# Optimization experiments

Measured on AMD Instinct MI355X. Metric: run time of the kernel, lower is better.

Reference implementation:

```python
import jax, jax.numpy as jnp
import numpy as np

N_DATASETS = 2
DATASET_CATS = (1536, 1536)
TOTAL_CATS = 3072
MAX_UNIFY = 1536
N_NODES = TOTAL_CATS + MAX_UNIFY  # 4608
LRELU_ALPHA = 0.2
BI_TEMP = 0.05
NEG_INF = -9e15


def setup_inputs() -> dict:
    key = jax.random.key(0)
    ks = jax.random.split(key, 12)
    nfeat, nfeat_out, nfeat_adj, nhid, nheads = 512, 256, 64, 64, 4
    att_out, mlp = 256, 512
    s = lambda k, sh: (jax.random.normal(k, sh, jnp.float32) * 0.05)
    return {
        'x': jax.random.normal(ks[0], (N_NODES, nfeat), jnp.float32),
        'W_before': s(ks[1], (nfeat, nfeat_out)),
        'b_before': jnp.zeros((nfeat_out,), jnp.float32),
        'W_adj': s(ks[2], (nfeat_out, nfeat_adj)),
        'b_adj': jnp.zeros((nfeat_adj,), jnp.float32),
        'W_heads': s(ks[3], (nheads, nfeat_out, nhid)),
        'a_heads': s(ks[4], (nheads, 2 * nhid)),
        'W_out': s(ks[5], (nheads * nhid, att_out)),
        'a_out': s(ks[6], (2 * att_out,)),
        'W_lin1': s(ks[7], (att_out, mlp)),
        'b_lin1': jnp.zeros((mlp,), jnp.float32),
    }


def _calc_adjacency(x_out, W_adj, b_adj):
    # linear_adj + L2 normalize + cosine similarity + row normalization via diag(1/rowsum)
    af = x_out @ W_adj + b_adj                              # [N, nfeat_adj]
    nrm = jnp.sqrt(jnp.sum(af * af, axis=1, keepdims=True))
    naf = af / jnp.maximum(nrm, 1e-12)
    sim = naf @ naf.T                                       # [N, N]
    rowsum = jnp.sum(sim, axis=1)
    r_inv = 1.0 / rowsum
    r_inv = jnp.where(jnp.isinf(r_inv), 0.0, r_inv)
    return r_inv[:, None] * sim                             # diag(1/rowsum) @ sim


def _gat_multihead(x, adj, W, a):
    # W: [H, F, d], a: [H, 2d]. Standard pyGAT dense attention, vectorized over heads.
    d = W.shape[-1]
    Wh = jnp.einsum('nf,hfd->hnd', x, W)                    # [H, N, d]
    f1 = jnp.einsum('hnd,hd->hn', Wh, a[:, :d])             # [H, N]
    f2 = jnp.einsum('hnd,hd->hn', Wh, a[:, d:])             # [H, N]
    e = jax.nn.leaky_relu(f1[:, :, None] + f2[:, None, :], LRELU_ALPHA)  # [H, N, N]
    att = jnp.where(adj[None] > 0, e, NEG_INF)
    att = jax.nn.softmax(att, axis=-1)
    return jnp.einsum('hnm,hmd->hnd', att, Wh)              # [H, N, d]


def _gat_single(x, adj, W, a):
    d = W.shape[-1]
    Wh = x @ W                                              # [N, d]
    f1 = Wh @ a[:d]
    f2 = Wh @ a[d:]
    e = jax.nn.leaky_relu(f1[:, None] + f2[None, :], LRELU_ALPHA)
    att = jnp.where(adj > 0, e, NEG_INF)
    att = jax.nn.softmax(att, axis=-1)
    return att @ Wh


def reference(x, W_before, b_before, W_adj, b_adj, W_heads, a_heads, W_out, a_out, W_lin1, b_lin1):
    x1 = x @ W_before + b_before                            # linear_before
    adj = _calc_adjacency(x1, W_adj, b_adj)                 # before relu, as in source
    x1 = jax.nn.relu(x1)
    # multi-head GAT layer 1 (concat=True -> elu per head, concat along feature dim)
    h = jax.nn.elu(_gat_multihead(x1, adj, W_heads, a_heads))   # [H, N, d]
    H, N, d = h.shape
    feat = jnp.transpose(h, (1, 0, 2)).reshape(N, H * d)
    x2 = feat + x1                                          # residual; dropout is eval no-op
    # output attention head (concat=False -> no elu inside)
    x3 = jax.nn.elu(_gat_single(x2, adj, W_out, a_out) + x2)
    feat_mlp = x3 @ W_lin1 + b_lin1                          # linear1
    # sep_bipartite_graphs: per-dataset column-softmax over unify columns
    bgs = []
    cur = 0
    for nc in DATASET_CATS:
        blk = adj[cur:cur + nc, TOTAL_CATS:]                 # [nc, MAX_UNIFY]
        bgs.append(jax.nn.softmax(blk / BI_TEMP, axis=0))
        cur += nc
    return (feat_mlp[TOTAL_CATS:],) + tuple(bgs)


if __name__ == '__main__':
    out = reference(**setup_inputs())
    for o in out:
        print(o.shape, o.dtype)
```

## Files before the change

kernel.cpp:

```cpp
#include <hip/hip_runtime.h>
#include <hip/hip_bf16.h>
#include <math.h>

constexpr int NTOT = 4608;
constexpr int TC   = 3072;
constexpr int MU   = 1536;
constexpr int NH   = 4;

constexpr long OFF_ADJ  = 0;
constexpr long OFF_X1   = OFF_ADJ  + (long)NTOT*NTOT;
constexpr long OFF_NAF  = OFF_X1   + (long)NTOT*256;
constexpr long OFF_PART = OFF_NAF  + (long)NTOT*64;
constexpr long OFF_RINV = OFF_PART + 72*64;
constexpr long OFF_WH   = OFF_RINV + NTOT;
constexpr long OFF_F1H  = OFF_WH   + (long)4*NTOT*64;
constexpr long OFF_F2H  = OFF_F1H  + (long)4*NTOT;
constexpr long OFF_MXH  = OFF_F2H  + (long)4*NTOT;
constexpr long OFF_CIH  = OFF_MXH  + (long)4*NTOT;
constexpr long OFF_X2   = OFF_CIH  + (long)4*NTOT;
constexpr long OFF_WH2  = OFF_X2   + (long)NTOT*256;
constexpr long OFF_F1S  = OFF_WH2  + (long)NTOT*256;
constexpr long OFF_F2S  = OFF_F1S  + NTOT;
constexpr long OFF_MXS  = OFF_F2S  + NTOT;
constexpr long OFF_CIS  = OFF_MXS  + NTOT;
constexpr long OFF_X3   = OFF_CIS  + NTOT;
constexpr long OFF_PMAX = OFF_X3   + (long)MU*256;
constexpr long OFF_PSUM = OFF_PMAX + (long)2*12*MU;
constexpr long OFF_FMAX = OFF_PSUM + (long)2*12*MU;
constexpr long OFF_FIS  = OFF_FMAX + (long)2*MU;
constexpr long OFF_L1   = OFF_FIS  + (long)2*MU;
constexpr long OFF_L2   = OFF_L1   + (long)4*NTOT;
constexpr long OFF_PARTS = OFF_ADJ + (long)TC*NTOT;
constexpr long OFF_POSB  = OFF_PARTS + 2L*NTOT*72;

typedef __attribute__((ext_vector_type(8))) short bf16x8;
typedef __attribute__((ext_vector_type(8))) unsigned short ushort8;
typedef __attribute__((ext_vector_type(4))) float floatx4;

__device__ __forceinline__ float lrelu(float x) { return (x >= 0.f) ? x : 0.2f * x; }
__device__ __forceinline__ float elu(float x)   { return (x > 0.f) ? x : expm1f(x); }
__device__ __forceinline__ unsigned short f2bf(float f) {
    unsigned u = __float_as_uint(f);
    u += 0x7FFFu + ((u >> 16) & 1u);
    return (unsigned short)(u >> 16);
}

__global__ __launch_bounds__(256) void zero_k(float* __restrict__ p)
{
    long idx = ((long)blockIdx.x * 256 + threadIdx.x) * 4;
    *(float4*)(p + idx) = make_float4(0.f, 0.f, 0.f, 0.f);
}

__global__ __launch_bounds__(256) void cvt_t(
    const float* __restrict__ in, unsigned short* __restrict__ out,
    int D, long inZ, long outZ)
{
    __shared__ float t[64][65];
    int n0 = blockIdx.x * 64, d0 = blockIdx.y * 64;
    const float* inz = in + (long)blockIdx.z * inZ;
    unsigned short* outz = out + (long)blockIdx.z * outZ;
    int tid = threadIdx.x;
    int r4 = tid >> 6, k = tid & 63;
    #pragma unroll
    for (int l = 0; l < 16; ++l) {
        int row = l * 4 + r4;
        t[row][k] = inz[(long)(n0 + row) * D + d0 + k];
    }
    __syncthreads();
    #pragma unroll
    for (int l = 0; l < 16; ++l) {
        int drow = l * 4 + r4;
        outz[(long)(d0 + drow) * NTOT + n0 + k] = f2bf(t[k][drow]);
    }
}

template<bool RELU_A, bool BIAS>
__global__ __launch_bounds__(256) void gemm_rm(
    const float* __restrict__ A, const float* __restrict__ B,
    const float* __restrict__ bias, float* __restrict__ C,
    int K, int M, long strideBz, long strideCz)
{
    __shared__ float As[16][68];
    __shared__ float Bs[16][68];
    const float* Bz = B + (long)blockIdx.z * strideBz;
    float* Cz = C + (long)blockIdx.z * strideCz;
    int tid = threadIdx.x;
    int r0 = blockIdx.x * 64;
    int c0 = blockIdx.y * 64;
    int ty = tid >> 4, tx = tid & 15;
    float acc[4][4] = {};
    for (int k0 = 0; k0 < K; k0 += 16) {
        #pragma unroll
        for (int l = 0; l < 4; ++l) {
            int idx = l * 256 + tid;
            int row = idx >> 4, kk = idx & 15;
            float v = A[(long)(r0 + row) * K + k0 + kk];
            if (RELU_A) v = fmaxf(v, 0.f);
            As[kk][row] = v;
        }
        #pragma unroll
        for (int l = 0; l < 4; ++l) {
            int idx = l * 256 + tid;
            int kk = idx >> 6, col = idx & 63;
            Bs[kk][col] = Bz[(long)(k0 + kk) * M + c0 + col];
        }
        __syncthreads();
        #pragma unroll
        for (int kk = 0; kk < 16; ++kk) {
            float av[4], bv[4];
            #pragma unroll
            for (int i = 0; i < 4; ++i) av[i] = As[kk][ty * 4 + i];
            #pragma unroll
            for (int j = 0; j < 4; ++j) bv[j] = Bs[kk][tx * 4 + j];
            #pragma unroll
            for (int i = 0; i < 4; ++i)
                #pragma unroll
                for (int j = 0; j < 4; ++j) acc[i][j] += av[i] * bv[j];
        }
        __syncthreads();
    }
    #pragma unroll
    for (int i = 0; i < 4; ++i) {
        int r = r0 + ty * 4 + i;
        #pragma unroll
        for (int j = 0; j < 4; ++j) {
            int c = c0 + tx * 4 + j;
            float v = acc[i][j];
            if (BIAS) v += bias[c];
            Cz[(long)r * M + c] = v;
        }
    }
}

__global__ __launch_bounds__(256) void af_naf(
    const float* __restrict__ x1, const float* __restrict__ W_adj,
    const float* __restrict__ b_adj, float* __restrict__ naf)
{
    __shared__ float rowbuf[4][256];
    int tid = threadIdx.x, w = tid >> 6, lane = tid & 63;
    int n = blockIdx.x * 4 + w;
    #pragma unroll
    for (int l = 0; l < 4; ++l) rowbuf[w][l * 64 + lane] = x1[(long)n * 256 + l * 64 + lane];
    __syncthreads();
    float acc = b_adj[lane];
    for (int k = 0; k < 256; ++k) acc += rowbuf[w][k] * W_adj[k * 64 + lane];
    float sq = acc * acc;
    #pragma unroll
    for (int off = 32; off >= 1; off >>= 1) sq += __shfl_xor(sq, off);
    float nrm = fmaxf(sqrtf(sq), 1e-12f);
    naf[(long)n * 64 + lane] = acc / nrm;
}

__global__ __launch_bounds__(256) void sim_k(
    const float* __restrict__ naf, float* __restrict__ sim,
    double* __restrict__ parts, unsigned long long* __restrict__ posb)
{
    __shared__ float As[64][68];
    __shared__ float Bs[64][68];
    __shared__ unsigned char sgn[64][16];
    int tid = threadIdx.x;
    int n0 = blockIdx.x * 64, m0 = blockIdx.y * 64;
    int row4 = tid >> 6, k = tid & 63;
    #pragma unroll
    for (int l = 0; l < 16; ++l) {
        int row = l * 4 + row4;
        As[k][row] = naf[(long)(n0 + row) * 64 + k];
        Bs[k][row] = naf[(long)(m0 + row) * 64 + k];
    }
    __syncthreads();
    int ty = tid >> 4, tx = tid & 15;
    float acc[4][4] = {};
    for (int kk = 0; kk < 64; ++kk) {
        float4 av = *(const float4*)&As[kk][ty * 4];
        float4 bv = *(const float4*)&Bs[kk][tx * 4];
        float a[4] = { av.x, av.y, av.z, av.w };
        float b[4] = { bv.x, bv.y, bv.z, bv.w };
        #pragma unroll
        for (int i = 0; i < 4; ++i)
            #pragma unroll
            for (int j = 0; j < 4; ++j) acc[i][j] += a[i] * b[j];
    }
    if (m0 >= TC && n0 < TC) {
        #pragma unroll
        for (int i = 0; i < 4; ++i) {
            long r = n0 + ty * 4 + i;
            float4 o = make_float4(acc[i][0], acc[i][1], acc[i][2], acc[i][3]);
            *(float4*)(sim + r * NTOT + m0 + tx * 4) = o;
        }
    }
    int mt = m0 >> 6;
    #pragma unroll
    for (int i = 0; i < 4; ++i) {
        double t = (double)acc[i][0] + (double)acc[i][1] + (double)acc[i][2] + (double)acc[i][3];
        #pragma unroll
        for (int off = 1; off < 16; off <<= 1) t += __shfl_xor(t, off);
        unsigned nib = (unsigned)(acc[i][0] > 0.f) | ((unsigned)(acc[i][1] > 0.f) << 1)
                     | ((unsigned)(acc[i][2] > 0.f) << 2) | ((unsigned)(acc[i][3] > 0.f) << 3);
        sgn[ty * 4 + i][tx] = (unsigned char)nib;
        if (tx == 0) parts[(long)(n0 + ty * 4 + i) * 72 + mt] = t;
    }
    __syncthreads();
    if (tid < 64) {
        unsigned long long w = 0;
        #pragma unroll
        for (int t = 0; t < 16; ++t)
            w |= (unsigned long long)sgn[tid][t] << (4 * t);
        posb[(long)(n0 + tid) * 72 + mt] = w;
    }
}

__global__ __launch_bounds__(256) void rowfin(
    const double* __restrict__ parts, const unsigned long long* __restrict__ posb,
    float* __restrict__ rinv, unsigned long long* __restrict__ maskb)
{
    int tid = threadIdx.x, w = tid >> 6, lane = tid & 63;
    int n = blockIdx.x * 4 + w;
    double s = parts[(long)n * 72 + lane];
    if (lane < 8) s += parts[(long)n * 72 + 64 + lane];
    #pragma unroll
    for (int off = 32; off >= 1; off >>= 1) s += __shfl_xor(s, off);
    float rs = (float)s;
    float r = 1.0f / rs;
    if (isinf(r)) r = 0.f;
    if (lane == 0) rinv[n] = r;
    unsigned long long pw = posb[(long)n * 72 + lane];
    unsigned long long mw = (r < 0.f) ? ~pw : pw;
    if (r == 0.f) mw = 0ull;
    maskb[(long)n * 72 + lane] = mw;
    if (lane < 8) {
        pw = posb[(long)n * 72 + 64 + lane];
        mw = (r < 0.f) ? ~pw : pw;
        if (r == 0.f) mw = 0ull;
        maskb[(long)n * 72 + 64 + lane] = mw;
    }
}

__global__ __launch_bounds__(256) void dots_k(
    const float* __restrict__ Wh, const float* __restrict__ a,
    float* __restrict__ f1, float* __restrict__ f2, int D)
{
    int tid = threadIdx.x, w = tid >> 6, lane = tid & 63;
    int n = blockIdx.x * 4 + w;
    int h = blockIdx.y;
    const float* row = Wh + ((long)h * NTOT + n) * D;
    const float* a1 = a + (long)h * 2 * D;
    const float* a2 = a1 + D;
    float p1 = 0.f, p2 = 0.f;
    for (int d = lane; d < D; d += 64) {
        float v = row[d];
        p1 += v * a1[d];
        p2 += v * a2[d];
    }
    #pragma unroll
    for (int off = 32; off >= 1; off >>= 1) { p1 += __shfl_xor(p1, off); p2 += __shfl_xor(p2, off); }
    if (lane == 0) { f1[(long)h * NTOT + n] = p1; f2[(long)h * NTOT + n] = p2; }
}

__global__ __launch_bounds__(256) void mh_attn(
    const unsigned long long* __restrict__ maskb,
    const float* __restrict__ f1, const float* __restrict__ f2,
    const unsigned short* __restrict__ Whbf, float* __restrict__ accb,
    float* __restrict__ lbuf)
{
    __shared__ unsigned short Ws[2][64][72];
    int tid = threadIdx.x;
    int wave = tid >> 6, lane = tid & 63;
    int n0 = blockIdx.x * 64;
    int h = blockIdx.y, ch = blockIdx.z;
    const float* f2h = f2 + (long)h * NTOT;
    const unsigned short* Wb = Whbf + (long)h * 64 * NTOT;
    int wd = tid >> 2, wc = (tid & 3) * 16;
    int arow = lane & 15, acol8 = (lane >> 4) * 8;
    int n = n0 + 16 * wave + arow;
    float r1 = f1[(long)h * NTOT + n];
    float lsum = 0.f;
    floatx4 acc[4] = {};
    int buf = 0;
    for (int mt = ch * 12; mt < ch * 12 + 12; ++mt) {
        int m0 = mt * 64;
        ushort8 wv0 = *(const ushort8*)&Wb[(long)wd * NTOT + m0 + wc];
        ushort8 wv1 = *(const ushort8*)&Wb[(long)wd * NTOT + m0 + wc + 8];
        unsigned long long mw = maskb[(long)n * 72 + mt];
        bf16x8 afr[2];
        #pragma unroll
        for (int ks = 0; ks < 2; ++ks) {
            int mc = m0 + ks * 32 + acol8;
            float4 fv0 = *(const float4*)(f2h + mc);
            float4 fv1 = *(const float4*)(f2h + mc + 4);
            unsigned bits = (unsigned)(mw >> (ks * 32 + acol8)) & 0xFFu;
            float f[8] = { fv0.x, fv0.y, fv0.z, fv0.w, fv1.x, fv1.y, fv1.z, fv1.w };
            #pragma unroll
            for (int j = 0; j < 8; ++j) {
                float s = r1 + f[j];
                float e = __expf(fmaxf(s, 0.2f * s));
                float p = ((bits >> j) & 1u) ? e : 0.f;
                lsum += p;
                afr[ks][j] = (short)f2bf(p);
            }
        }
        *(ushort8*)&Ws[buf][wd][wc] = wv0;
        *(ushort8*)&Ws[buf][wd][wc + 8] = wv1;
        __syncthreads();
        #pragma unroll
        for (int ks = 0; ks < 2; ++ks) {
            #pragma unroll
            for (int dt = 0; dt < 4; ++dt) {
                bf16x8 bfr = *(bf16x8*)&Ws[buf][16 * dt + arow][ks * 32 + acol8];
                acc[dt] = __builtin_amdgcn_mfma_f32_16x16x32_bf16(afr[ks], bfr, acc[dt], 0, 0, 0);
            }
        }
        buf ^= 1;
    }
    lsum += __shfl_xor(lsum, 16);
    lsum += __shfl_xor(lsum, 32);
    if (lane < 16) atomicAdd(lbuf + (long)h * NTOT + n0 + 16 * wave + lane, lsum);
    int crow = n0 + 16 * wave + (lane >> 4) * 4;
    int ccol = h * 64 + (lane & 15);
    #pragma unroll
    for (int dt = 0; dt < 4; ++dt)
        #pragma unroll
        for (int r = 0; r < 4; ++r)
            atomicAdd(accb + (long)(crow + r) * 256 + ccol + dt * 16, acc[dt][r]);
}

__global__ __launch_bounds__(256) void mh_fin(
    const float* __restrict__ accb, const float* __restrict__ lbuf,
    const float* __restrict__ x1, float* __restrict__ x2)
{
    long idx = ((long)blockIdx.x * 256 + threadIdx.x) * 4;
    long r = idx >> 8;
    int h = (int)((idx & 255) >> 6);
    float l = lbuf[(long)h * NTOT + r];
    float inv = (l > 0.f) ? 1.0f / l : 0.f;
    float4 a = *(const float4*)(accb + idx);
    float4 xv = *(const float4*)(x1 + idx);
    float4 o;
    o.x = elu(a.x * inv) + fmaxf(xv.x, 0.f);
    o.y = elu(a.y * inv) + fmaxf(xv.y, 0.f);
    o.z = elu(a.z * inv) + fmaxf(xv.z, 0.f);
    o.w = elu(a.w * inv) + fmaxf(xv.w, 0.f);
    *(float4*)(x2 + idx) = o;
}

__global__ __launch_bounds__(256) void s_attn(
    const unsigned long long* __restrict__ maskb,
    const float* __restrict__ f1, const float* __restrict__ f2,
    const unsigned short* __restrict__ Wh2bf, float* __restrict__ accb,
    float* __restrict__ lbuf)
{
    __shared__ unsigned short Ws[2][64][72];
    int tid = threadIdx.x;
    int wave = tid >> 6, lane = tid & 63;
    int lr0 = blockIdx.x * 32;
    int c0 = blockIdx.y * 64;
    int ch = blockIdx.z;
    int wd = tid >> 2, wc = (tid & 3) * 16;
    int arow = lane & 15, acol8 = (lane >> 4) * 8;
    int rt = wave & 1;
    int dt0 = (wave >> 1) * 2;
    int n = TC + lr0 + 16 * rt + arow;
    float r1 = f1[n];
    float lsum = 0.f;
    floatx4 acc[2] = {};
    int buf = 0;
    for (int mt = ch * 12; mt < ch * 12 + 12; ++mt) {
        int m0 = mt * 64;
        ushort8 wv0 = *(const ushort8*)&Wh2bf[(long)(c0 + wd) * NTOT + m0 + wc];
        ushort8 wv1 = *(const ushort8*)&Wh2bf[(long)(c0 + wd) * NTOT + m0 + wc + 8];
        unsigned long long mw = maskb[(long)n * 72 + mt];
        bf16x8 afr[2];
        #pragma unroll
        for (int ks = 0; ks < 2; ++ks) {
            int mc = m0 + ks * 32 + acol8;
            float4 fv0 = *(const float4*)(f2 + mc);
            float4 fv1 = *(const float4*)(f2 + mc + 4);
            unsigned bits = (unsigned)(mw >> (ks * 32 + acol8)) & 0xFFu;
            float f[8] = { fv0.x, fv0.y, fv0.z, fv0.w, fv1.x, fv1.y, fv1.z, fv1.w };
            #pragma unroll
            for (int j = 0; j < 8; ++j) {
                float s = r1 + f[j];
                float e = __expf(fmaxf(s, 0.2f * s));
                float p = ((bits >> j) & 1u) ? e : 0.f;
                lsum += p;
                afr[ks][j] = (short)f2bf(p);
            }
        }
        *(ushort8*)&Ws[buf][wd][wc] = wv0;
        *(ushort8*)&Ws[buf][wd][wc + 8] = wv1;
        __syncthreads();
        #pragma unroll
        for (int ks = 0; ks < 2; ++ks) {
            #pragma unroll
            for (int t = 0; t < 2; ++t) {
                bf16x8 bfr = *(bf16x8*)&Ws[buf][16 * (dt0 + t) + arow][ks * 32 + acol8];
                acc[t] = __builtin_amdgcn_mfma_f32_16x16x32_bf16(afr[ks], bfr, acc[t], 0, 0, 0);
            }
        }
        buf ^= 1;
    }
    lsum += __shfl_xor(lsum, 16);
    lsum += __shfl_xor(lsum, 32);
    if (blockIdx.y == 0 && wave < 2 && lane < 16)
        atomicAdd(lbuf + lr0 + 16 * wave + lane, lsum);
    int crow = lr0 + 16 * rt + (lane >> 4) * 4;
    int ccol = c0 + (lane & 15);
    #pragma unroll
    for (int t = 0; t < 2; ++t)
        #pragma unroll
        for (int r = 0; r < 4; ++r)
            atomicAdd(accb + (long)(crow + r) * 256 + ccol + (dt0 + t) * 16, acc[t][r]);
}

__global__ __launch_bounds__(256) void s_fin(
    const float* __restrict__ accb, const float* __restrict__ lbuf,
    const float* __restrict__ x2, float* __restrict__ x3)
{
    long idx = ((long)blockIdx.x * 256 + threadIdx.x) * 4;
    long r = idx >> 8;
    float l = lbuf[r];
    float inv = (l > 0.f) ? 1.0f / l : 0.f;
    float4 a = *(const float4*)(accb + idx);
    float4 xv = *(const float4*)(x2 + (long)TC * 256 + idx);
    float4 o;
    o.x = elu(a.x * inv + xv.x);
    o.y = elu(a.y * inv + xv.y);
    o.z = elu(a.z * inv + xv.z);
    o.w = elu(a.w * inv + xv.w);
    *(float4*)(x3 + idx) = o;
}

__global__ __launch_bounds__(256) void bi_partial(
    const float* __restrict__ sim, const float* __restrict__ rinv,
    float* __restrict__ pmax, float* __restrict__ psum)
{
    int c = blockIdx.x * 256 + threadIdx.x;
    int ch = blockIdx.y;
    int ds = blockIdx.z;
    float m = -3.0e38f, s = 0.f;
    int rbase = ds * MU + ch * 128;
    for (int r = 0; r < 128; ++r) {
        float a = sim[(long)(rbase + r) * NTOT + TC + c] * rinv[rbase + r];
        float v = a * 20.0f;
        if (v <= m) s += expf(v - m);
        else { s = s * expf(m - v) + 1.f; m = v; }
    }
    pmax[((long)ds * 12 + ch) * MU + c] = m;
    psum[((long)ds * 12 + ch) * MU + c] = s;
}

__global__ __launch_bounds__(256) void bi_combine(
    const float* __restrict__ pmax, const float* __restrict__ psum,
    float* __restrict__ fmax, float* __restrict__ fis)
{
    int b = blockIdx.x;
    int ds = b / 6, ct = b % 6;
    int c = ct * 256 + threadIdx.x;
    float m = -3.0e38f;
    for (int ch = 0; ch < 12; ++ch) m = fmaxf(m, pmax[((long)ds * 12 + ch) * MU + c]);
    float s = 0.f;
    for (int ch = 0; ch < 12; ++ch)
        s += psum[((long)ds * 12 + ch) * MU + c] * expf(pmax[((long)ds * 12 + ch) * MU + c] - m);
    fmax[ds * MU + c] = m;
    fis[ds * MU + c] = 1.0f / s;
}

__global__ __launch_bounds__(256) void bi_norm(
    const float* __restrict__ sim, const float* __restrict__ rinv,
    const float* __restrict__ fmax, const float* __restrict__ fis,
    float* __restrict__ outbg)
{
    int c = blockIdx.x * 256 + threadIdx.x;
    int ch = blockIdx.y;
    int ds = blockIdx.z;
    float m = fmax[ds * MU + c], inv = fis[ds * MU + c];
    long obase = (long)ds * MU * MU;
    int rbase = ch * 128;
    for (int r = 0; r < 128; ++r) {
        int row = ds * MU + rbase + r;
        float a = sim[(long)row * NTOT + TC + c] * rinv[row];
        float v = a * 20.0f;
        outbg[obase + (long)(rbase + r) * MU + c] = expf(v - m) * inv;
    }
}

extern "C" void kernel_launch(void* const* d_in, const int* in_sizes, int n_in,
                              void* d_out, int out_size, void* d_ws, size_t ws_size,
                              hipStream_t stream)
{
    const float* x        = (const float*)d_in[0];
    const float* W_before = (const float*)d_in[1];
    const float* b_before = (const float*)d_in[2];
    const float* W_adj    = (const float*)d_in[3];
    const float* b_adj    = (const float*)d_in[4];
    const float* W_heads  = (const float*)d_in[5];
    const float* a_heads  = (const float*)d_in[6];
    const float* W_out    = (const float*)d_in[7];
    const float* a_out    = (const float*)d_in[8];
    const float* W_lin1   = (const float*)d_in[9];
    const float* b_lin1   = (const float*)d_in[10];
    float* out = (float*)d_out;
    float* ws  = (float*)d_ws;

    float* sim  = ws + OFF_ADJ;
    float* x1p  = ws + OFF_X1;
    float* naf  = ws + OFF_NAF;
    float* rinv = ws + OFF_RINV;
    float* Wh   = ws + OFF_WH;
    float* f1h  = ws + OFF_F1H;
    float* f2h  = ws + OFF_F2H;
    float* x2   = ws + OFF_X2;
    float* Wh2  = ws + OFF_WH2;
    float* f1s  = ws + OFF_F1S;
    float* f2s  = ws + OFF_F2S;
    float* x3   = ws + OFF_X3;
    float* pmax = ws + OFF_PMAX;
    float* psum = ws + OFF_PSUM;
    float* fmx  = ws + OFF_FMAX;
    float* fis  = ws + OFF_FIS;
    float* l1   = ws + OFF_L1;
    float* l2   = ws + OFF_L2;
    float* acc1 = ws + OFF_WH2;
    float* acc2 = ws + OFF_X1;
    unsigned short* Whbf  = (unsigned short*)(ws + OFF_X2);
    unsigned short* Wh2bf = (unsigned short*)(ws + OFF_X1 + (long)MU * 256);
    unsigned long long* maskb = (unsigned long long*)(ws + OFF_WH);
    double* parts = (double*)(ws + OFF_PARTS);
    unsigned long long* posb = (unsigned long long*)(ws + OFF_POSB);

    dim3 b256(256);

    zero_k<<<dim3(NTOT * 256 / 1024), b256, 0, stream>>>(acc1);
    zero_k<<<dim3(20), b256, 0, stream>>>(l1);
    gemm_rm<false, true><<<dim3(72, 4, 1), b256, 0, stream>>>(x, W_before, b_before, x1p, 512, 256, 0, 0);
    af_naf<<<dim3(1152), b256, 0, stream>>>(x1p, W_adj, b_adj, naf);
    sim_k<<<dim3(72, 72), b256, 0, stream>>>(naf, sim, parts, posb);
    gemm_rm<true, false><<<dim3(72, 1, 4), b256, 0, stream>>>(x1p, W_heads, nullptr, Wh, 256, 64,
                                                              (long)256 * 64, (long)NTOT * 64);
    cvt_t<<<dim3(72, 1, 4), b256, 0, stream>>>(Wh, Whbf, 64, (long)NTOT * 64, (long)64 * NTOT);
    dots_k<<<dim3(1152, 4), b256, 0, stream>>>(Wh, a_heads, f1h, f2h, 64);
    rowfin<<<dim3(1152), b256, 0, stream>>>(parts, posb, rinv, maskb);
    mh_attn<<<dim3(72, 4, 6), b256, 0, stream>>>(maskb, f1h, f2h, Whbf, acc1, l1);
    mh_fin<<<dim3(NTOT * 256 / 1024), b256, 0, stream>>>(acc1, l1, x1p, x2);
    zero_k<<<dim3(MU * 256 / 1024), b256, 0, stream>>>(acc2);
    gemm_rm<false, false><<<dim3(72, 4, 1), b256, 0, stream>>>(x2, W_out, nullptr, Wh2, 256, 256, 0, 0);
    cvt_t<<<dim3(72, 4, 1), b256, 0, stream>>>(Wh2, Wh2bf, 256, 0, 0);
    dots_k<<<dim3(1152, 1), b256, 0, stream>>>(Wh2, a_out, f1s, f2s, 256);
    s_attn<<<dim3(48, 4, 6), b256, 0, stream>>>(maskb, f1s, f2s, Wh2bf, acc2, l2);
    s_fin<<<dim3(MU * 256 / 1024), b256, 0, stream>>>(acc2, l2, x2, x3);
    gemm_rm<false, true><<<dim3(24, 8, 1), b256, 0, stream>>>(x3, W_lin1, b_lin1, out, 256, 512, 0, 0);
    bi_partial<<<dim3(6, 12, 2), b256, 0, stream>>>(sim, rinv, pmax, psum);
    bi_combine<<<dim3(12), b256, 0, stream>>>(pmax, psum, fmx, fis);
    bi_norm<<<dim3(6, 12, 2), b256, 0, stream>>>(sim, rinv, fmx, fis, out + (long)MU * 512);
}
```

Before: 401.3 us.

## Enlarge similarity GEMM tiles to 128x128 with transposed normalized features

The cosine-similarity kernel now computes 128x128 output tiles with an 8x8 register micro-tile per thread, cutting the grid from 72x72 to 36x36 blocks. The normalized adjacency features are stored transposed so tile loads are coalesced, the B tile is padded to avoid bank conflicts, and row-sum partials shrink to 36 per row. The generic GEMM also gets float4 global loads for A and float4 shared reads. The larger accumulator raises register pressure, which may lower occupancy.

```diff
diff --git a/kernel.cpp b/kernel.cpp
--- a/kernel.cpp
+++ b/kernel.cpp
@@ -88,15 +88,19 @@
     int r0 = blockIdx.x * 64;
     int c0 = blockIdx.y * 64;
     int ty = tid >> 4, tx = tid & 15;
+    int srow = tid >> 2, skg = tid & 3;
     float acc[4][4] = {};
     for (int k0 = 0; k0 < K; k0 += 16) {
-        #pragma unroll
-        for (int l = 0; l < 4; ++l) {
-            int idx = l * 256 + tid;
-            int row = idx >> 4, kk = idx & 15;
-            float v = A[(long)(r0 + row) * K + k0 + kk];
-            if (RELU_A) v = fmaxf(v, 0.f);
-            As[kk][row] = v;
+        {
+            float4 v = *(const float4*)&A[(long)(r0 + srow) * K + k0 + skg * 4];
+            if (RELU_A) {
+                v.x = fmaxf(v.x, 0.f); v.y = fmaxf(v.y, 0.f);
+                v.z = fmaxf(v.z, 0.f); v.w = fmaxf(v.w, 0.f);
+            }
+            As[skg * 4 + 0][srow] = v.x;
+            As[skg * 4 + 1][srow] = v.y;
+            As[skg * 4 + 2][srow] = v.z;
+            As[skg * 4 + 3][srow] = v.w;
         }
         #pragma unroll
         for (int l = 0; l < 4; ++l) {
@@ -107,15 +111,14 @@
         __syncthreads();
         #pragma unroll
         for (int kk = 0; kk < 16; ++kk) {
-            float av[4], bv[4];
-            #pragma unroll
-            for (int i = 0; i < 4; ++i) av[i] = As[kk][ty * 4 + i];
-            #pragma unroll
-            for (int j = 0; j < 4; ++j) bv[j] = Bs[kk][tx * 4 + j];
+            float4 av = *(const float4*)&As[kk][ty * 4];
+            float4 bv = *(const float4*)&Bs[kk][tx * 4];
+            float a[4] = { av.x, av.y, av.z, av.w };
+            float b[4] = { bv.x, bv.y, bv.z, bv.w };
             #pragma unroll
             for (int i = 0; i < 4; ++i)
                 #pragma unroll
-                for (int j = 0; j < 4; ++j) acc[i][j] += av[i] * bv[j];
+                for (int j = 0; j < 4; ++j) acc[i][j] += a[i] * b[j];
         }
         __syncthreads();
     }
@@ -134,7 +137,7 @@
 
 __global__ __launch_bounds__(256) void af_naf(
     const float* __restrict__ x1, const float* __restrict__ W_adj,
-    const float* __restrict__ b_adj, float* __restrict__ naf)
+    const float* __restrict__ b_adj, float* __restrict__ nafT)
 {
     __shared__ float rowbuf[4][256];
     int tid = threadIdx.x, w = tid >> 6, lane = tid & 63;
@@ -148,64 +151,73 @@
     #pragma unroll
     for (int off = 32; off >= 1; off >>= 1) sq += __shfl_xor(sq, off);
     float nrm = fmaxf(sqrtf(sq), 1e-12f);
-    naf[(long)n * 64 + lane] = acc / nrm;
+    nafT[(long)lane * NTOT + n] = acc / nrm;
 }
 
 __global__ __launch_bounds__(256) void sim_k(
-    const float* __restrict__ naf, float* __restrict__ sim,
+    const float* __restrict__ nafT, float* __restrict__ sim,
     double* __restrict__ parts, unsigned long long* __restrict__ posb)
 {
-    __shared__ float As[64][68];
-    __shared__ float Bs[64][68];
-    __shared__ unsigned char sgn[64][16];
+    __shared__ float As[64][132];
+    __shared__ float Bs[64][140];
+    __shared__ unsigned char sgn[128][16];
     int tid = threadIdx.x;
-    int n0 = blockIdx.x * 64, m0 = blockIdx.y * 64;
-    int row4 = tid >> 6, k = tid & 63;
-    #pragma unroll
-    for (int l = 0; l < 16; ++l) {
-        int row = l * 4 + row4;
-        As[k][row] = naf[(long)(n0 + row) * 64 + k];
-        Bs[k][row] = naf[(long)(m0 + row) * 64 + k];
+    int n0 = blockIdx.x * 128, m0 = blockIdx.y * 128;
+    #pragma unroll
+    for (int l = 0; l < 32; ++l) {
+        int flat = l * 256 + tid;
+        int k = flat >> 7, r = flat & 127;
+        As[k][r] = nafT[(long)k * NTOT + n0 + r];
+        Bs[k][r + ((r >> 5) << 2)] = nafT[(long)k * NTOT + m0 + r];
     }
     __syncthreads();
     int ty = tid >> 4, tx = tid & 15;
-    float acc[4][4] = {};
+    int cp = tx * 8 + ((tx >> 2) << 2);
+    float acc[8][8] = {};
     for (int kk = 0; kk < 64; ++kk) {
-        float4 av = *(const float4*)&As[kk][ty * 4];
-        float4 bv = *(const float4*)&Bs[kk][tx * 4];
-        float a[4] = { av.x, av.y, av.z, av.w };
-        float b[4] = { bv.x, bv.y, bv.z, bv.w };
-        #pragma unroll
-        for (int i = 0; i < 4; ++i)
+        float4 a0 = *(const float4*)&As[kk][ty * 8];
+        float4 a1 = *(const float4*)&As[kk][ty * 8 + 4];
+        float4 b0 = *(const float4*)&Bs[kk][cp];
+        float4 b1 = *(const float4*)&Bs[kk][cp + 4];
+        float a[8] = { a0.x, a0.y, a0.z, a0.w, a1.x, a1.y, a1.z, a1.w };
+        float b[8] = { b0.x, b0.y, b0.z, b0.w, b1.x, b1.y, b1.z, b1.w };
+        #pragma unroll
+        for (int i = 0; i < 8; ++i)
             #pragma unroll
-            for (int j = 0; j < 4; ++j) acc[i][j] += a[i] * b[j];
+            for (int j = 0; j < 8; ++j) acc[i][j] += a[i] * b[j];
     }
     if (m0 >= TC && n0 < TC) {
         #pragma unroll
-        for (int i = 0; i < 4; ++i) {
-            long r = n0 + ty * 4 + i;
-            float4 o = make_float4(acc[i][0], acc[i][1], acc[i][2], acc[i][3]);
-            *(float4*)(sim + r * NTOT + m0 + tx * 4) = o;
-        }
-    }
-    int mt = m0 >> 6;
-    #pragma unroll
-    for (int i = 0; i < 4; ++i) {
-        double t = (double)acc[i][0] + (double)acc[i][1] + (double)acc[i][2] + (double)acc[i][3];
+        for (int i = 0; i < 8; ++i) {
+            long r = n0 + ty * 8 + i;
+            float4 o0 = make_float4(acc[i][0], acc[i][1], acc[i][2], acc[i][3]);
+            float4 o1 = make_float4(acc[i][4], acc[i][5], acc[i][6], acc[i][7]);
+            *(float4*)(sim + r * NTOT + m0 + tx * 8) = o0;
+            *(float4*)(sim + r * NTOT + m0 + tx * 8 + 4) = o1;
+        }
+    }
+    #pragma unroll
+    for (int i = 0; i < 8; ++i) {
+        double t = ((double)acc[i][0] + (double)acc[i][1]) + ((double)acc[i][2] + (double)acc[i][3])
+                 + ((double)acc[i][4] + (double)acc[i][5]) + ((double)acc[i][6] + (double)acc[i][7]);
         #pragma unroll
         for (int off = 1; off < 16; off <<= 1) t += __shfl_xor(t, off);
-        unsigned nib = (unsigned)(acc[i][0] > 0.f) | ((unsigned)(acc[i][1] > 0.f) << 1)
-                     | ((unsigned)(acc[i][2] > 0.f) << 2) | ((unsigned)(acc[i][3] > 0.f) << 3);
-        sgn[ty * 4 + i][tx] = (unsigned char)nib;
-        if (tx == 0) parts[(long)(n0 + ty * 4 + i) * 72 + mt] = t;
+        unsigned byte = 0;
+        #pragma unroll
+        for (int j = 0; j < 8; ++j) byte |= (unsigned)(acc[i][j] > 0.f) << j;
+        sgn[ty * 8 + i][tx] = (unsigned char)byte;
+        if (tx == 0) parts[(long)(n0 + ty * 8 + i) * 36 + blockIdx.y] = t;
     }
     __syncthreads();
-    if (tid < 64) {
-        unsigned long long w = 0;
-        #pragma unroll
-        for (int t = 0; t < 16; ++t)
-            w |= (unsigned long long)sgn[tid][t] << (4 * t);
-        posb[(long)(n0 + tid) * 72 + mt] = w;
+    if (tid < 128) {
+        unsigned long long w0 = 0, w1 = 0;
+        #pragma unroll
+        for (int t = 0; t < 8; ++t) {
+            w0 |= (unsigned long long)sgn[tid][t] << (8 * t);
+            w1 |= (unsigned long long)sgn[tid][8 + t] << (8 * t);
+        }
+        posb[(long)(n0 + tid) * 72 + 2 * blockIdx.y] = w0;
+        posb[(long)(n0 + tid) * 72 + 2 * blockIdx.y + 1] = w1;
     }
 }
 
@@ -215,8 +227,7 @@
 {
     int tid = threadIdx.x, w = tid >> 6, lane = tid & 63;
     int n = blockIdx.x * 4 + w;
-    double s = parts[(long)n * 72 + lane];
-    if (lane < 8) s += parts[(long)n * 72 + 64 + lane];
+    double s = (lane < 36) ? parts[(long)n * 36 + lane] : 0.0;
     #pragma unroll
     for (int off = 32; off >= 1; off >>= 1) s += __shfl_xor(s, off);
     float rs = (float)s;
@@ -503,7 +514,7 @@
 
     float* sim  = ws + OFF_ADJ;
     float* x1p  = ws + OFF_X1;
-    float* naf  = ws + OFF_NAF;
+    float* nafT = ws + OFF_NAF;
     float* rinv = ws + OFF_RINV;
     float* Wh   = ws + OFF_WH;
     float* f1h  = ws + OFF_F1H;
@@ -532,8 +543,8 @@
     zero_k<<<dim3(NTOT * 256 / 1024), b256, 0, stream>>>(acc1);
     zero_k<<<dim3(20), b256, 0, stream>>>(l1);
     gemm_rm<false, true><<<dim3(72, 4, 1), b256, 0, stream>>>(x, W_before, b_before, x1p, 512, 256, 0, 0);
-    af_naf<<<dim3(1152), b256, 0, stream>>>(x1p, W_adj, b_adj, naf);
-    sim_k<<<dim3(72, 72), b256, 0, stream>>>(naf, sim, parts, posb);
+    af_naf<<<dim3(1152), b256, 0, stream>>>(x1p, W_adj, b_adj, nafT);
+    sim_k<<<dim3(36, 36), b256, 0, stream>>>(nafT, sim, parts, posb);
     gemm_rm<true, false><<<dim3(72, 1, 4), b256, 0, stream>>>(x1p, W_heads, nullptr, Wh, 256, 64,
                                                               (long)256 * 64, (long)NTOT * 64);
     cvt_t<<<dim3(72, 1, 4), b256, 0, stream>>>(Wh, Whbf, 64, (long)NTOT * 64, (long)64 * NTOT);
```

Result: no change. 399.2 us (-0.5%).

## Exploit similarity symmetry in sim_k and vectorize GEMM tile loads

Applied to the files above, without the earlier changes.

The cosine-similarity kernel now launches only upper-triangular tile pairs. Each tile also emits the transposed row-sum partials and positivity bitmasks for the mirrored tile, which roughly halves the N×N matmul work. The normalized features are stored transposed so the tile loads in sim_k are coalesced. The generic GEMM now loads A with float4 and reads shared memory with vector loads. This adds shared-memory buffers and a triangular index decode, and changes summation order slightly.

```diff
diff --git a/kernel.cpp b/kernel.cpp
--- a/kernel.cpp
+++ b/kernel.cpp
@@ -88,15 +88,19 @@
     int r0 = blockIdx.x * 64;
     int c0 = blockIdx.y * 64;
     int ty = tid >> 4, tx = tid & 15;
+    int srow = tid >> 2, skg = tid & 3;
     float acc[4][4] = {};
     for (int k0 = 0; k0 < K; k0 += 16) {
-        #pragma unroll
-        for (int l = 0; l < 4; ++l) {
-            int idx = l * 256 + tid;
-            int row = idx >> 4, kk = idx & 15;
-            float v = A[(long)(r0 + row) * K + k0 + kk];
-            if (RELU_A) v = fmaxf(v, 0.f);
-            As[kk][row] = v;
+        {
+            float4 v = *(const float4*)&A[(long)(r0 + srow) * K + k0 + skg * 4];
+            if (RELU_A) {
+                v.x = fmaxf(v.x, 0.f); v.y = fmaxf(v.y, 0.f);
+                v.z = fmaxf(v.z, 0.f); v.w = fmaxf(v.w, 0.f);
+            }
+            As[skg * 4 + 0][srow] = v.x;
+            As[skg * 4 + 1][srow] = v.y;
+            As[skg * 4 + 2][srow] = v.z;
+            As[skg * 4 + 3][srow] = v.w;
         }
         #pragma unroll
         for (int l = 0; l < 4; ++l) {
@@ -107,15 +111,14 @@
         __syncthreads();
         #pragma unroll
         for (int kk = 0; kk < 16; ++kk) {
-            float av[4], bv[4];
-            #pragma unroll
-            for (int i = 0; i < 4; ++i) av[i] = As[kk][ty * 4 + i];
-            #pragma unroll
-            for (int j = 0; j < 4; ++j) bv[j] = Bs[kk][tx * 4 + j];
+            float4 av = *(const float4*)&As[kk][ty * 4];
+            float4 bv = *(const float4*)&Bs[kk][tx * 4];
+            float a[4] = { av.x, av.y, av.z, av.w };
+            float b[4] = { bv.x, bv.y, bv.z, bv.w };
             #pragma unroll
             for (int i = 0; i < 4; ++i)
                 #pragma unroll
-                for (int j = 0; j < 4; ++j) acc[i][j] += av[i] * bv[j];
+                for (int j = 0; j < 4; ++j) acc[i][j] += a[i] * b[j];
         }
         __syncthreads();
     }
@@ -134,7 +137,7 @@
 
 __global__ __launch_bounds__(256) void af_naf(
     const float* __restrict__ x1, const float* __restrict__ W_adj,
-    const float* __restrict__ b_adj, float* __restrict__ naf)
+    const float* __restrict__ b_adj, float* __restrict__ nafT)
 {
     __shared__ float rowbuf[4][256];
     int tid = threadIdx.x, w = tid >> 6, lane = tid & 63;
@@ -148,24 +151,31 @@
     #pragma unroll
     for (int off = 32; off >= 1; off >>= 1) sq += __shfl_xor(sq, off);
     float nrm = fmaxf(sqrtf(sq), 1e-12f);
-    naf[(long)n * 64 + lane] = acc / nrm;
+    nafT[(long)lane * NTOT + n] = acc / nrm;
 }
 
 __global__ __launch_bounds__(256) void sim_k(
-    const float* __restrict__ naf, float* __restrict__ sim,
+    const float* __restrict__ nafT, float* __restrict__ sim,
     double* __restrict__ parts, unsigned long long* __restrict__ posb)
 {
     __shared__ float As[64][68];
     __shared__ float Bs[64][68];
-    __shared__ unsigned char sgn[64][16];
+    __shared__ unsigned char sgnR[64][16];
+    __shared__ unsigned char sgnC[64][16];
+    __shared__ double csd[16][65];
+    int idx = blockIdx.x;
+    int bi = (int)(72.5 - sqrt(72.5 * 72.5 - 2.0 * (double)idx));
+    while ((bi + 1) * 72 - ((bi + 1) * bi) / 2 <= idx) ++bi;
+    while (bi * 72 - (bi * (bi - 1)) / 2 > idx) --bi;
+    int bj = bi + (idx - (bi * 72 - (bi * (bi - 1)) / 2));
+    int n0 = bi * 64, m0 = bj * 64;
     int tid = threadIdx.x;
-    int n0 = blockIdx.x * 64, m0 = blockIdx.y * 64;
     int row4 = tid >> 6, k = tid & 63;
     #pragma unroll
     for (int l = 0; l < 16; ++l) {
         int row = l * 4 + row4;
-        As[k][row] = naf[(long)(n0 + row) * 64 + k];
-        Bs[k][row] = naf[(long)(m0 + row) * 64 + k];
+        As[k][row] = nafT[(long)k * NTOT + n0 + row];
+        Bs[k][row] = nafT[(long)k * NTOT + m0 + row];
     }
     __syncthreads();
     int ty = tid >> 4, tx = tid & 15;
@@ -180,7 +190,7 @@
             #pragma unroll
             for (int j = 0; j < 4; ++j) acc[i][j] += a[i] * b[j];
     }
-    if (m0 >= TC && n0 < TC) {
+    if (n0 < TC && m0 >= TC) {
         #pragma unroll
         for (int i = 0; i < 4; ++i) {
             long r = n0 + ty * 4 + i;
@@ -188,24 +198,44 @@
             *(float4*)(sim + r * NTOT + m0 + tx * 4) = o;
         }
     }
-    int mt = m0 >> 6;
     #pragma unroll
     for (int i = 0; i < 4; ++i) {
-        double t = (double)acc[i][0] + (double)acc[i][1] + (double)acc[i][2] + (double)acc[i][3];
+        double t = ((double)acc[i][0] + (double)acc[i][1]) + ((double)acc[i][2] + (double)acc[i][3]);
         #pragma unroll
         for (int off = 1; off < 16; off <<= 1) t += __shfl_xor(t, off);
         unsigned nib = (unsigned)(acc[i][0] > 0.f) | ((unsigned)(acc[i][1] > 0.f) << 1)
                      | ((unsigned)(acc[i][2] > 0.f) << 2) | ((unsigned)(acc[i][3] > 0.f) << 3);
-        sgn[ty * 4 + i][tx] = (unsigned char)nib;
-        if (tx == 0) parts[(long)(n0 + ty * 4 + i) * 72 + mt] = t;
+        sgnR[ty * 4 + i][tx] = (unsigned char)nib;
+        if (tx == 0) parts[(long)(n0 + ty * 4 + i) * 72 + bj] = t;
+    }
+    if (bi != bj) {
+        #pragma unroll
+        for (int j = 0; j < 4; ++j) {
+            double cd = ((double)acc[0][j] + (double)acc[1][j]) + ((double)acc[2][j] + (double)acc[3][j]);
+            csd[ty][tx * 4 + j] = cd;
+            unsigned nib = (unsigned)(acc[0][j] > 0.f) | ((unsigned)(acc[1][j] > 0.f) << 1)
+                         | ((unsigned)(acc[2][j] > 0.f) << 2) | ((unsigned)(acc[3][j] > 0.f) << 3);
+            sgnC[tx * 4 + j][ty] = (unsigned char)nib;
+        }
     }
     __syncthreads();
     if (tid < 64) {
         unsigned long long w = 0;
         #pragma unroll
         for (int t = 0; t < 16; ++t)
-            w |= (unsigned long long)sgn[tid][t] << (4 * t);
-        posb[(long)(n0 + tid) * 72 + mt] = w;
+            w |= (unsigned long long)sgnR[tid][t] << (4 * t);
+        posb[(long)(n0 + tid) * 72 + bj] = w;
+        if (bi != bj) {
+            double s = 0.0;
+            #pragma unroll
+            for (int t = 0; t < 16; ++t) s += csd[t][tid];
+            parts[(long)(m0 + tid) * 72 + bi] = s;
+            unsigned long long wc = 0;
+            #pragma unroll
+            for (int t = 0; t < 16; ++t)
+                wc |= (unsigned long long)sgnC[tid][t] << (4 * t);
+            posb[(long)(m0 + tid) * 72 + bi] = wc;
+        }
     }
 }
 
@@ -503,7 +533,7 @@
 
     float* sim  = ws + OFF_ADJ;
     float* x1p  = ws + OFF_X1;
-    float* naf  = ws + OFF_NAF;
+    float* nafT = ws + OFF_NAF;
     float* rinv = ws + OFF_RINV;
     float* Wh   = ws + OFF_WH;
     float* f1h  = ws + OFF_F1H;
@@ -532,8 +562,8 @@
     zero_k<<<dim3(NTOT * 256 / 1024), b256, 0, stream>>>(acc1);
     zero_k<<<dim3(20), b256, 0, stream>>>(l1);
     gemm_rm<false, true><<<dim3(72, 4, 1), b256, 0, stream>>>(x, W_before, b_before, x1p, 512, 256, 0, 0);
-    af_naf<<<dim3(1152), b256, 0, stream>>>(x1p, W_adj, b_adj, naf);
-    sim_k<<<dim3(72, 72), b256, 0, stream>>>(naf, sim, parts, posb);
+    af_naf<<<dim3(1152), b256, 0, stream>>>(x1p, W_adj, b_adj, nafT);
+    sim_k<<<dim3(2628), b256, 0, stream>>>(nafT, sim, parts, posb);
     gemm_rm<true, false><<<dim3(72, 1, 4), b256, 0, stream>>>(x1p, W_heads, nullptr, Wh, 256, 64,
                                                               (long)256 * 64, (long)NTOT * 64);
     cvt_t<<<dim3(72, 1, 4), b256, 0, stream>>>(Wh, Whbf, 64, (long)NTOT * 64, (long)64 * NTOT);
```

Measured after the change: 406.1 us. No clear change (+1.2%).
